# Performance work log

Hardware: AMD Instinct MI355X
Metric: run time of the kernel (lower is better)

The kernel has to match this reference:

```python
import jax, jax.numpy as jnp
import numpy as np

T = 2048          # tokens (single-sequence prefill)
HID = 4096        # hidden_size
NH = 32           # num attention heads
NKV = 8           # num kv heads (GQA)
HD = 128          # head_dim
QKV_OUT = (NH + 2 * NKV) * HD  # 6144
THETA = 10000.0
SCALING = HD ** -0.5


def setup_inputs() -> dict:
    key = jax.random.key(0)
    ks = jax.random.split(key, 8)
    positions = jnp.arange(T, dtype=jnp.int32)
    # per-token int8 quantized hidden states (symmetric, [-127,127])
    q_act = jax.random.randint(ks[0], (T, HID), -127, 128, dtype=jnp.int32)
    # per-token dynamic activation scale
    act_scale = jax.random.uniform(ks[1], (T,), jnp.float32) * 0.01 + 0.001
    # int4 weights stored unsigned [0,15] with per-output-channel scale & zero point
    w_qkv_q = jax.random.randint(ks[2], (QKV_OUT, HID), 0, 16, dtype=jnp.int32)
    w_qkv_scale = jax.random.uniform(ks[3], (QKV_OUT,), jnp.float32) * 0.01 + 0.001
    w_qkv_zero = jax.random.uniform(ks[4], (QKV_OUT,), jnp.float32) * 2.0 + 7.0
    w_o_q = jax.random.randint(ks[5], (HID, HID), 0, 16, dtype=jnp.int32)
    w_o_scale = jax.random.uniform(ks[6], (HID,), jnp.float32) * 0.01 + 0.001
    w_o_zero = jax.random.uniform(ks[7], (HID,), jnp.float32) * 2.0 + 7.0
    return dict(positions=positions, q_act=q_act, act_scale=act_scale,
                w_qkv_q=w_qkv_q, w_qkv_scale=w_qkv_scale, w_qkv_zero=w_qkv_zero,
                w_o_q=w_o_q, w_o_scale=w_o_scale, w_o_zero=w_o_zero)


def w4a8_linear(qa_f, s_a, a_sum, qw, s_w, z_w):
    # y[t,o] = s_a[t]*s_w[o] * ( (qa @ qw^T)[t,o] - z_w[o]*sum_j qa[t,j] )
    acc = jnp.matmul(qa_f, qw.astype(jnp.float32).T)  # [T, O]
    return (s_a[:, None] * s_w[None, :]) * (acc - z_w[None, :] * a_sum[:, None])


def apply_rope(x, positions):
    # neox-style RoPE over full head_dim
    half = HD // 2
    inv_freq = THETA ** (-jnp.arange(0, half, dtype=jnp.float32) / half * 1.0)
    inv_freq = 1.0 / (THETA ** (jnp.arange(0, HD, 2, dtype=jnp.float32) / HD))
    freqs = positions.astype(jnp.float32)[:, None] * inv_freq[None, :]  # [T, HD/2]
    cos = jnp.cos(freqs)[:, None, :]
    sin = jnp.sin(freqs)[:, None, :]
    x1, x2 = x[..., :half], x[..., half:]
    return jnp.concatenate([x1 * cos - x2 * sin, x2 * cos + x1 * sin], axis=-1)


def dynamic_quant_with_sum(x):
    # per-token symmetric int8 dynamic quantization + fused sum
    s = jnp.maximum(jnp.max(jnp.abs(x), axis=-1), 1e-8) / 127.0  # [T]
    q = jnp.clip(jnp.round(x / s[:, None]), -127, 127)
    return q, s, jnp.sum(q, axis=-1)


def reference(positions, q_act, act_scale, w_qkv_q, w_qkv_scale, w_qkv_zero,
              w_o_q, w_o_scale, w_o_zero):
    qa_f = q_act.astype(jnp.float32)
    a_sum = jnp.sum(qa_f, axis=-1)  # fused activation sum
    qkv = w4a8_linear(qa_f, act_scale, a_sum, w_qkv_q, w_qkv_scale, w_qkv_zero)
    q, k, v = jnp.split(qkv, [NH * HD, NH * HD + NKV * HD], axis=-1)
    q = q.reshape(T, NH, HD)
    k = k.reshape(T, NKV, HD)
    v = v.reshape(T, NKV, HD)
    q = apply_rope(q, positions)
    k = apply_rope(k, positions)
    # GQA: repeat kv heads
    rep = NH // NKV
    k = jnp.repeat(k, rep, axis=1)  # [T, NH, HD]
    v = jnp.repeat(v, rep, axis=1)
    scores = jnp.einsum('qhd,khd->hqk', q, k) * SCALING  # [NH, T, T]
    causal = jnp.tril(jnp.ones((T, T), dtype=bool))
    scores = jnp.where(causal[None], scores, -jnp.inf)
    probs = jax.nn.softmax(scores, axis=-1)
    attn = jnp.einsum('hqk,khd->qhd', probs, v).reshape(T, NH * HD)
    # invoke_quant_fuse_sum: dynamic per-token quantization of attn output
    q2, s2, sum2 = dynamic_quant_with_sum(attn)
    out = w4a8_linear(q2, s2, sum2, w_o_q, w_o_scale, w_o_zero)
    return out
```

## Files before the change

### kernel.cpp

```cpp
#include <hip/hip_runtime.h>

#define T 2048
#define HID 4096
#define NH 32
#define NKV 8
#define HD 128
#define QKV_OUT ((NH + 2*NKV) * HD)
#define SCALING 0.08838834764831843f
#define QS2 0.12751744954f
#define DEFER_THR 10.0f
#define ROPE_C 0.20762050593046014f

typedef __attribute__((ext_vector_type(8))) short bfrag;
typedef __attribute__((ext_vector_type(4))) float ffrag;
typedef __attribute__((ext_vector_type(4))) int  ifrag;
typedef __attribute__((ext_vector_type(16))) char c16;

__device__ __forceinline__ short f2bf(float f) {
  unsigned u = __builtin_bit_cast(unsigned, f);
  u += 0x7fffu + ((u >> 16) & 1u);
  return (short)(u >> 16);
}

__device__ __forceinline__ void split2(float x, short& hi, short& lo) {
  unsigned u = __builtin_bit_cast(unsigned, x);
  unsigned uh = u + (0x7fffu + ((u >> 16) & 1u));
  hi = (short)(uh >> 16);
  float fh = __builtin_bit_cast(float, uh & 0xffff0000u);
  float r = x - fh;
  unsigned ur = __builtin_bit_cast(unsigned, r);
  ur += 0x7fffu + ((ur >> 16) & 1u);
  lo = (short)(ur >> 16);
}

__device__ __forceinline__ void gload_lds16(const void* g, void* l) {
  __builtin_amdgcn_global_load_lds(
      (const __attribute__((address_space(1))) unsigned int*)g,
      (__attribute__((address_space(3))) unsigned int*)l, 16, 0, 0);
}


__global__ __launch_bounds__(256)
void asum_conv(const int* __restrict__ qact, float* __restrict__ a_sum,
               char* __restrict__ a_i8, float2* __restrict__ tab) {
  __shared__ int red[256];
  const int t = blockIdx.x, tid = threadIdx.x;
  if (t < 512) {
    int idx = t * 256 + tid;
    int p = idx >> 6, j = idx & 63;
    float fr = (float)p * exp2f(-ROPE_C * (float)j);
    float sn, cs; sincosf(fr, &sn, &cs);
    tab[idx] = make_float2(cs, sn);
  }
  const int* row = qact + (size_t)t * HID + tid * 16;
  int s = 0;
  c16 o;
#pragma unroll
  for (int i = 0; i < 4; i++) {
    int4 v = *(const int4*)(row + i * 4);
    s += v.x + v.y + v.z + v.w;
    o[i*4+0] = (char)v.x; o[i*4+1] = (char)v.y;
    o[i*4+2] = (char)v.z; o[i*4+3] = (char)v.w;
  }
  const int chunk = (tid & ~7) | ((tid & 7) ^ (t & 7));
  *(c16*)(a_i8 + (size_t)t * HID + chunk * 16) = o;
  red[tid] = s; __syncthreads();
  for (int off = 128; off > 0; off >>= 1) {
    if (tid < off) red[tid] += red[tid + off];
    __syncthreads();
  }
  if (tid == 0) a_sum[t] = (float)red[0];
}

__global__ __launch_bounds__(256)
void conv_i2c(const int* __restrict__ src, char* __restrict__ dst, int n16) {
  int idx = blockIdx.x * 256 + threadIdx.x;
  if (idx >= n16) return;
  const int4* s4 = (const int4*)src + (size_t)idx * 4;
  c16 o;
#pragma unroll
  for (int j = 0; j < 4; j++) {
    int4 v = s4[j];
    o[j*4+0] = (char)v.x; o[j*4+1] = (char)v.y;
    o[j*4+2] = (char)v.z; o[j*4+3] = (char)v.w;
  }
  const int idxp = (idx & ~7) | ((idx & 7) ^ ((idx >> 8) & 7));
  *(c16*)(dst + (size_t)idxp * 16) = o;
}

__global__ __launch_bounds__(256)
void gemm_i8(const char* __restrict__ A, const char* __restrict__ W,
             const float* __restrict__ s_a, const float* __restrict__ asum,
             const float* __restrict__ s_w, const float* __restrict__ z_w,
             float* __restrict__ C, int M, int N, int K) {
  __shared__ __align__(16) char As[2][128 * 128];
  __shared__ __align__(16) char Bs[2][128 * 128];
  const int tid = threadIdx.x;
  const int lane = tid & 63;
  const int quad = lane >> 4, l15 = lane & 15;
  const int wave = tid >> 6;
  const int wm = (wave >> 1) * 64, wn = (wave & 1) * 64;
  const int bm = blockIdx.y * 128, bn = blockIdx.x * 128;
  const int sr = tid >> 3, sc = (tid & 7) * 16;

  ifrag acc[4][4];
#pragma unroll
  for (int mi = 0; mi < 4; mi++)
#pragma unroll
    for (int ni = 0; ni < 4; ni++)
      acc[mi][ni] = (ifrag){0, 0, 0, 0};

  auto stage = [&](int k0, int b) {
#pragma unroll
    for (int j = 0; j < 4; j++) {
      gload_lds16(A + (size_t)(bm + j * 32 + sr) * K + k0 + sc,
                  &As[b][j * 4096 + tid * 16]);
      gload_lds16(W + (size_t)(bn + j * 32 + sr) * K + k0 + sc,
                  &Bs[b][j * 4096 + tid * 16]);
    }
  };

  const int scol0 = ((quad)     ^ (l15 & 7)) * 16;
  const int scol1 = ((4 + quad) ^ (l15 & 7)) * 16;

  stage(0, 0);
  asm volatile("s_waitcnt vmcnt(0)" ::: "memory");
  __builtin_amdgcn_s_barrier();

  int cur = 0;
  for (int k0 = 0; k0 < K; k0 += 128) {
    if (k0 + 128 < K) stage(k0 + 128, cur ^ 1);

#pragma unroll
    for (int ks = 0; ks < 2; ks++) {
      const int scol = ks ? scol1 : scol0;
      ifrag af[4], bfv[4];
#pragma unroll
      for (int mi = 0; mi < 4; mi++)
        af[mi] = *(const ifrag*)&As[cur][(wm + mi * 16 + l15) * 128 + scol];
#pragma unroll
      for (int ni = 0; ni < 4; ni++)
        bfv[ni] = *(const ifrag*)&Bs[cur][(wn + ni * 16 + l15) * 128 + scol];
#pragma unroll
      for (int mi = 0; mi < 4; mi++)
#pragma unroll
        for (int ni = 0; ni < 4; ni++)
          acc[mi][ni] = __builtin_amdgcn_mfma_i32_16x16x64_i8(
              af[mi], bfv[ni], acc[mi][ni], 0, 0, 0);
    }

    asm volatile("s_waitcnt vmcnt(0)" ::: "memory");
    __builtin_amdgcn_s_barrier();
    cur ^= 1;
  }

#pragma unroll
  for (int mi = 0; mi < 4; mi++) {
    int row0 = bm + wm + mi * 16 + quad * 4;
#pragma unroll
    for (int r = 0; r < 4; r++) {
      int row = row0 + r;
      float sa = s_a[row], av = asum[row];
#pragma unroll
      for (int ni = 0; ni < 4; ni++) {
        int col = bn + wn + ni * 16 + l15;
        C[(size_t)row * N + col] = (sa * s_w[col]) * ((float)acc[mi][ni][r] - z_w[col] * av);
      }
    }
  }
}

__global__ __launch_bounds__(256)
void split_kv(const float* __restrict__ qkv, const int* __restrict__ positions,
              const float2* __restrict__ tab,
              short* __restrict__ Kh, short* __restrict__ Kl,
              short* __restrict__ Vth) {
  __shared__ __align__(16) short Vh_lds[128 * 72];
  const int kvh = blockIdx.y;
  const int t0 = blockIdx.x * 64;
  const int tid = threadIdx.x;

#pragma unroll
  for (int it = 0; it < 4; it++) {
    int c = tid + 256 * it;
    int key = c >> 4, dc = c & 15;
    const int t = t0 + key;
    const float* kr = qkv + (size_t)t * QKV_OUT
                      + (size_t)NH * HD + (size_t)kvh * HD;
    float4 a = *(const float4*)(kr + dc * 4);
    float4 b = *(const float4*)(kr + dc * 4 + 64);
    float av[4] = {a.x, a.y, a.z, a.w};
    float bv[4] = {b.x, b.y, b.z, b.w};
    const float2* tr = tab + (size_t)positions[t] * 64 + dc * 4;
    short4 ha, la, hb, lb;
    short hh, ll;
#pragma unroll
    for (int jj = 0; jj < 4; jj++) {
      float cs = tr[jj].x, sn = tr[jj].y;
      float x1 = av[jj], x2 = bv[jj];
      float r1 = x1 * cs - x2 * sn;
      float r2 = x2 * cs + x1 * sn;
      split2(r1, hh, ll); ((short*)&ha)[jj] = hh; ((short*)&la)[jj] = ll;
      split2(r2, hh, ll); ((short*)&hb)[jj] = hh; ((short*)&lb)[jj] = ll;
    }
    const int uu = ((dc >> 1) ^ t) & 7;
    const int h4 = (dc & 1) * 4;
    size_t base = (size_t)kvh * T * HD + (size_t)t * HD;
    *(short4*)(Kh + base + uu * 8 + h4) = ha;
    *(short4*)(Kl + base + uu * 8 + h4) = la;
    *(short4*)(Kh + base + (8 + uu) * 8 + h4) = hb;
    *(short4*)(Kl + base + (8 + uu) * 8 + h4) = lb;
  }
#pragma unroll
  for (int i = 0; i < 8; i++) {
    int c = tid + 256 * i;
    int key = c >> 5, dc = c & 31;
    float4 f = *(const float4*)(qkv + (size_t)(t0 + key) * QKV_OUT
                                + (size_t)(NH + NKV) * HD + (size_t)kvh * HD + dc * 4);
    Vh_lds[(dc*4+0)*72 + key] = f2bf(f.x);
    Vh_lds[(dc*4+1)*72 + key] = f2bf(f.y);
    Vh_lds[(dc*4+2)*72 + key] = f2bf(f.z);
    Vh_lds[(dc*4+3)*72 + key] = f2bf(f.w);
  }
  __syncthreads();
#pragma unroll
  for (int i = 0; i < 2; i++) {
    int c = tid + 256 * i;
    int row = c >> 2, cc = c & 3;
    int sd = (row >> 1) & 3;
    size_t o = (size_t)kvh * HD * T + (size_t)row * T + t0 + ((cc ^ sd)) * 8;
    *(bfrag*)(Vth + o) = *(const bfrag*)&Vh_lds[row * 72 + cc * 8];
  }
#pragma unroll
  for (int i = 0; i < 2; i++) {
    int c = tid + 256 * i;
    int row = c >> 2, cc = c & 3;
    int sd = (row >> 1) & 3;
    size_t o = (size_t)kvh * HD * T + (size_t)row * T + t0 + 32 + ((cc ^ sd)) * 8;
    *(bfrag*)(Vth + o) = *(const bfrag*)&Vh_lds[row * 72 + 32 + cc * 8];
  }
}

__global__ __launch_bounds__(256)
void attn_kernel(const float* __restrict__ qkv, const int* __restrict__ positions,
                 const float2* __restrict__ tab,
                 const short* __restrict__ Kh, const short* __restrict__ Kl,
                 const short* __restrict__ Vth,
                 float* __restrict__ attn) {
  __shared__ __align__(16) short Ksh[2][32 * 128];
  __shared__ __align__(16) short Ksl[2][32 * 128];
  __shared__ __align__(16) short Vsh[2][128 * 32];
  __shared__ __align__(16) short Psh[4 * 16 * 40];

  const int kvh = blockIdx.x & 7;
  const int pair = blockIdx.x >> 3;
  const int tid = threadIdx.x;
  const int lane = tid & 63;
  const int wv = tid >> 6;
  const int l15 = lane & 15, quad = lane >> 4;
  const int h = kvh * 4 + wv;
  short* Pw = Psh + wv * 16 * 40;

  const short* KhB = Kh + (size_t)kvh * T * HD;
  const short* KlB = Kl + (size_t)kvh * T * HD;
  const short* VhB = Vth + (size_t)kvh * HD * T;

  const int offK0 = (tid >> 4) * 128 + (tid & 15) * 8;
  const int offK1 = offK0 + 16 * 128;
  const int offV0 = (tid >> 2) * T + (tid & 3) * 8;
  const int offV1 = offV0 + 64 * T;
  const int wv1k = wv * 1024;

  auto stage = [&](int k0, int b) {
    const short* khs = KhB + (size_t)k0 * HD;
    const short* kls = KlB + (size_t)k0 * HD;
    const short* vs  = VhB + k0;
    gload_lds16(khs + offK0, (char*)&Ksh[b][0] + wv1k);
    gload_lds16(khs + offK1, (char*)&Ksh[b][0] + 4096 + wv1k);
    gload_lds16(kls + offK0, (char*)&Ksl[b][0] + wv1k);
    gload_lds16(kls + offK1, (char*)&Ksl[b][0] + 4096 + wv1k);
    gload_lds16(vs + offV0, (char*)&Vsh[b][0] + wv1k);
    gload_lds16(vs + offV1, (char*)&Vsh[b][0] + 4096 + wv1k);
  };

  const int sdv = (l15 >> 1) & 3;
  const int vq8 = (quad ^ sdv) * 8;
  int uuk[4];
#pragma unroll
  for (int kc = 0; kc < 4; kc++) {
    int s = 4 * kc + quad;
    uuk[kc] = ((s & 8) | ((s ^ l15) & 7)) * 8;
  }

  bfrag ones;
#pragma unroll
  for (int j = 0; j < 8; j++) ones[j] = (short)0x3f80;

  for (int pass = 0; pass < 2; pass++) {
    const int qt = pass ? pair : 127 - pair;
    const int q0 = qt * 16;
    const int nk = (q0 >> 5) + 1;

    bfrag qh[4], ql[4];
    {
      const float* qrow = qkv + (size_t)(q0 + l15) * QKV_OUT + (size_t)h * HD;
      float fvv[4][8];
#pragma unroll
      for (int kc = 0; kc < 4; kc++) {
        float4 f0 = *(const float4*)(qrow + kc * 32 + quad * 8);
        float4 f1 = *(const float4*)(qrow + kc * 32 + quad * 8 + 4);
        fvv[kc][0] = f0.x; fvv[kc][1] = f0.y; fvv[kc][2] = f0.z; fvv[kc][3] = f0.w;
        fvv[kc][4] = f1.x; fvv[kc][5] = f1.y; fvv[kc][6] = f1.z; fvv[kc][7] = f1.w;
      }
      const float2* trw = tab + (size_t)positions[q0 + l15] * 64;
#pragma unroll
      for (int kc = 0; kc < 2; kc++) {
#pragma unroll
        for (int j = 0; j < 8; j++) {
          int d = kc * 32 + quad * 8 + j;
          float2 cssn = trw[d];
          float x1 = fvv[kc][j], x2 = fvv[kc + 2][j];
          fvv[kc][j]     = x1 * cssn.x - x2 * cssn.y;
          fvv[kc + 2][j] = x2 * cssn.x + x1 * cssn.y;
        }
      }
#pragma unroll
      for (int kc = 0; kc < 4; kc++)
#pragma unroll
        for (int j = 0; j < 8; j++) {
          short hi, lo; split2(fvv[kc][j] * QS2, hi, lo);
          qh[kc][j] = hi; ql[kc][j] = lo;
        }
    }

    ffrag o[8], ol;
    ol = (ffrag){0.f, 0.f, 0.f, 0.f};
#pragma unroll
    for (int n = 0; n < 8; n++) o[n] = (ffrag){0.f, 0.f, 0.f, 0.f};
    float m_i[4] = {-1e30f, -1e30f, -1e30f, -1e30f};

    auto compute_tile = [&](int k0, int b, bool maskq) {
      const short* ksh = &Ksh[b][0];
      const short* ksl = &Ksl[b][0];
      const short* vsh = &Vsh[b][0];
      ffrag s[2];
      s[0] = (ffrag){0.f,0.f,0.f,0.f}; s[1] = (ffrag){0.f,0.f,0.f,0.f};
#pragma unroll
      for (int kc = 0; kc < 4; kc++) {
#pragma unroll
        for (int n = 0; n < 2; n++) {
          const int rb = (n * 16 + l15) * 128 + uuk[kc];
          bfrag bh = *(const bfrag*)&ksh[rb];
          bfrag bl = *(const bfrag*)&ksl[rb];
          s[n] = __builtin_amdgcn_mfma_f32_16x16x32_bf16(qh[kc], bh, s[n], 0,0,0);
          s[n] = __builtin_amdgcn_mfma_f32_16x16x32_bf16(qh[kc], bl, s[n], 0,0,0);
          s[n] = __builtin_amdgcn_mfma_f32_16x16x32_bf16(ql[kc], bh, s[n], 0,0,0);
        }
      }
      float sv[2][4];
#pragma unroll
      for (int n = 0; n < 2; n++)
#pragma unroll
        for (int r = 0; r < 4; r++) {
          float v = s[n][r];
          if (maskq) {
            int key = k0 + n * 16 + l15;
            int row = q0 + quad * 4 + r;
            if (key > row) v = -1e30f;
          }
          sv[n][r] = v;
        }
      float lm[4];
      bool trig = false;
#pragma unroll
      for (int r = 0; r < 4; r++) {
        lm[r] = fmaxf(sv[0][r], sv[1][r]);
        trig = trig || (lm[r] > m_i[r] + DEFER_THR);
      }
      if (__any(trig)) {
#pragma unroll
        for (int r = 0; r < 4; r++) {
          float m2 = lm[r];
          m2 = fmaxf(m2, __shfl_xor(m2, 1));
          m2 = fmaxf(m2, __shfl_xor(m2, 2));
          m2 = fmaxf(m2, __shfl_xor(m2, 4));
          m2 = fmaxf(m2, __shfl_xor(m2, 8));
          float mn = fmaxf(m_i[r], m2);
          float a = exp2f(m_i[r] - mn);
          m_i[r] = mn;
          ol[r] *= a;
#pragma unroll
          for (int n = 0; n < 8; n++) o[n][r] *= a;
        }
      }
#pragma unroll
      for (int n = 0; n < 2; n++)
#pragma unroll
        for (int r = 0; r < 4; r++) {
          float p = exp2f(sv[n][r] - m_i[r]);
          Pw[(quad*4 + r) * 40 + n*16 + l15] = f2bf(p);
        }
      bfrag ph = *(const bfrag*)&Pw[l15 * 40 + quad * 8];
      ol = __builtin_amdgcn_mfma_f32_16x16x32_bf16(ph, ones, ol, 0,0,0);
#pragma unroll
      for (int n = 0; n < 8; n++) {
        bfrag vh = *(const bfrag*)&vsh[(n * 16 + l15) * 32 + vq8];
        o[n] = __builtin_amdgcn_mfma_f32_16x16x32_bf16(ph, vh, o[n], 0,0,0);
      }
    };

    stage(0, 0);
    asm volatile("s_waitcnt vmcnt(0)" ::: "memory");
    __builtin_amdgcn_s_barrier();

    int cur = 0;
    for (int kt = 0; kt < nk - 1; kt++) {
      const int k0 = kt << 5;
      stage(k0 + 32, cur ^ 1);
      compute_tile(k0, cur, false);
      asm volatile("s_waitcnt vmcnt(0)" ::: "memory");
      __builtin_amdgcn_s_barrier();
      cur ^= 1;
    }
    compute_tile((nk - 1) << 5, cur, true);
    __builtin_amdgcn_s_barrier();

    float inv[4];
#pragma unroll
    for (int r = 0; r < 4; r++) inv[r] = 1.f / ol[r];
#pragma unroll
    for (int n = 0; n < 8; n++)
#pragma unroll
      for (int r = 0; r < 4; r++) {
        int row = q0 + quad * 4 + r;
        attn[(size_t)row * HID + (size_t)h * HD + n * 16 + l15] = o[n][r] * inv[r];
      }
  }
}

__global__ __launch_bounds__(256)
void quant_kernel(const float* __restrict__ x, char* __restrict__ q2,
                  float* __restrict__ s2, float* __restrict__ sum2) {
  __shared__ float red[256];
  const int t = blockIdx.x, tid = threadIdx.x;
  const float* row = x + (size_t)t * HID;
  float4 v[4];
  float m = 0.f;
#pragma unroll
  for (int i = 0; i < 4; i++) {
    v[i] = *(const float4*)(row + tid * 16 + i * 4);
    m = fmaxf(m, fmaxf(fmaxf(fabsf(v[i].x), fabsf(v[i].y)),
                       fmaxf(fabsf(v[i].z), fabsf(v[i].w))));
  }
  red[tid] = m; __syncthreads();
  for (int off = 128; off > 0; off >>= 1) {
    if (tid < off) red[tid] = fmaxf(red[tid], red[tid + off]);
    __syncthreads();
  }
  float s = fmaxf(red[0], 1e-8f) / 127.f;
  __syncthreads();
  float ssum = 0.f;
  c16 o;
#pragma unroll
  for (int i = 0; i < 4; i++) {
    float q;
    q = fminf(127.f, fmaxf(-127.f, rintf(v[i].x / s))); ssum += q; o[i*4+0] = (char)(int)q;
    q = fminf(127.f, fmaxf(-127.f, rintf(v[i].y / s))); ssum += q; o[i*4+1] = (char)(int)q;
    q = fminf(127.f, fmaxf(-127.f, rintf(v[i].z / s))); ssum += q; o[i*4+2] = (char)(int)q;
    q = fminf(127.f, fmaxf(-127.f, rintf(v[i].w / s))); ssum += q; o[i*4+3] = (char)(int)q;
  }
  const int chunk = (tid & ~7) | ((tid & 7) ^ (t & 7));
  *(c16*)(q2 + (size_t)t * HID + chunk * 16) = o;
  red[tid] = ssum; __syncthreads();
  for (int off = 128; off > 0; off >>= 1) {
    if (tid < off) red[tid] += red[tid + off];
    __syncthreads();
  }
  if (tid == 0) { s2[t] = s; sum2[t] = red[0]; }
}

extern "C" void kernel_launch(void* const* d_in, const int* in_sizes, int n_in,
                              void* d_out, int out_size, void* d_ws, size_t ws_size,
                              hipStream_t stream) {
  const int*   positions   = (const int*)d_in[0];
  const int*   q_act       = (const int*)d_in[1];
  const float* act_scale   = (const float*)d_in[2];
  const int*   w_qkv_q     = (const int*)d_in[3];
  const float* w_qkv_scale = (const float*)d_in[4];
  const float* w_qkv_zero  = (const float*)d_in[5];
  const int*   w_o_q       = (const int*)d_in[6];
  const float* w_o_scale   = (const float*)d_in[7];
  const float* w_o_zero    = (const float*)d_in[8];
  float* out = (float*)d_out;

  size_t off = 0;
  auto alloc = [&](size_t bytes) -> void* {
    void* p = (char*)d_ws + off;
    off += (bytes + 255) & ~(size_t)255;
    return p;
  };
  float* qkv   = (float*)alloc((size_t)T * QKV_OUT * 4);
  char*  act8  = (char*)alloc((size_t)T * HID);
  char*  w8    = (char*)alloc((size_t)QKV_OUT * HID);
  short* Kh    = (short*)alloc((size_t)NKV * T * HD * 2);
  short* Kl    = (short*)alloc((size_t)NKV * T * HD * 2);
  short* Vth   = (short*)alloc((size_t)NKV * T * HD * 2);
  float* a_sum = (float*)alloc(T * 4);
  float* s2    = (float*)alloc(T * 4);
  float* sum2  = (float*)alloc(T * 4);
  float2* tab  = (float2*)alloc((size_t)T * 64 * 8);
  (void)ws_size;

  asum_conv<<<T, 256, 0, stream>>>(q_act, a_sum, act8, tab);
  conv_i2c<<<(QKV_OUT * HID / 16 + 255) / 256, 256, 0, stream>>>(
      w_qkv_q, w8, QKV_OUT * HID / 16);
  gemm_i8<<<dim3(QKV_OUT / 128, T / 128), 256, 0, stream>>>(
      act8, w8, act_scale, a_sum, w_qkv_scale, w_qkv_zero, qkv, T, QKV_OUT, HID);
  split_kv<<<dim3(T / 64, NKV), 256, 0, stream>>>(
      qkv, positions, tab, Kh, Kl, Vth);
  attn_kernel<<<dim3(512), 256, 0, stream>>>(
      qkv, positions, tab, Kh, Kl, Vth, out);
  conv_i2c<<<(HID * HID / 16 + 255) / 256, 256, 0, stream>>>(
      w_o_q, w8, HID * HID / 16);
  quant_kernel<<<T, 256, 0, stream>>>(out, act8, s2, sum2);
  gemm_i8<<<dim3(HID / 128, T / 128), 256, 0, stream>>>(
      act8, w8, s2, sum2, w_o_scale, w_o_zero, out, T, HID, HID);
}
```

Before: 467.0 us.

## Fold weight conversions into prep kernels and split attention into single-tile blocks

Both int32-to-int8 weight conversion launches are removed. Their blocks are appended to the activation-prep kernel and to the K/V split kernel, so each conversion runs alongside other memory-bound work instead of as its own launch. The attention kernel no longer has each block process a paired long and short query tile in two passes. It now launches 1024 blocks, one query tile each, ordered heaviest first. This aims to cut launch count and serial gaps and improve scheduling granularity, but it gives up the explicit pairwise load balancing and relies on the hardware block scheduler.

```diff
diff --git a/kernel.cpp b/kernel.cpp
--- a/kernel.cpp
+++ b/kernel.cpp
@@ -41,10 +41,28 @@
 
 
 __global__ __launch_bounds__(256)
-void asum_conv(const int* __restrict__ qact, float* __restrict__ a_sum,
-               char* __restrict__ a_i8, float2* __restrict__ tab) {
+void prep_a(const int* __restrict__ qact, float* __restrict__ a_sum,
+            char* __restrict__ a_i8, float2* __restrict__ tab,
+            const int* __restrict__ wsrc, char* __restrict__ wdst) {
   __shared__ int red[256];
-  const int t = blockIdx.x, tid = threadIdx.x;
+  const int bid = blockIdx.x, tid = threadIdx.x;
+
+  if (bid >= T) {
+    int idx = (bid - T) * 256 + tid;
+    const int4* s4 = (const int4*)wsrc + (size_t)idx * 4;
+    c16 o;
+#pragma unroll
+    for (int j = 0; j < 4; j++) {
+      int4 v = s4[j];
+      o[j*4+0] = (char)v.x; o[j*4+1] = (char)v.y;
+      o[j*4+2] = (char)v.z; o[j*4+3] = (char)v.w;
+    }
+    const int idxp = (idx & ~7) | ((idx & 7) ^ ((idx >> 8) & 7));
+    *(c16*)(wdst + (size_t)idxp * 16) = o;
+    return;
+  }
+
+  const int t = bid;
   if (t < 512) {
     int idx = t * 256 + tid;
     int p = idx >> 6, j = idx & 63;
@@ -70,22 +88,6 @@
     __syncthreads();
   }
   if (tid == 0) a_sum[t] = (float)red[0];
-}
-
-__global__ __launch_bounds__(256)
-void conv_i2c(const int* __restrict__ src, char* __restrict__ dst, int n16) {
-  int idx = blockIdx.x * 256 + threadIdx.x;
-  if (idx >= n16) return;
-  const int4* s4 = (const int4*)src + (size_t)idx * 4;
-  c16 o;
-#pragma unroll
-  for (int j = 0; j < 4; j++) {
-    int4 v = s4[j];
-    o[j*4+0] = (char)v.x; o[j*4+1] = (char)v.y;
-    o[j*4+2] = (char)v.z; o[j*4+3] = (char)v.w;
-  }
-  const int idxp = (idx & ~7) | ((idx & 7) ^ ((idx >> 8) & 7));
-  *(c16*)(dst + (size_t)idxp * 16) = o;
 }
 
 __global__ __launch_bounds__(256)
@@ -171,14 +173,31 @@
 }
 
 __global__ __launch_bounds__(256)
-void split_kv(const float* __restrict__ qkv, const int* __restrict__ positions,
-              const float2* __restrict__ tab,
-              short* __restrict__ Kh, short* __restrict__ Kl,
-              short* __restrict__ Vth) {
+void kv_prep(const float* __restrict__ qkv, const int* __restrict__ positions,
+             const float2* __restrict__ tab,
+             short* __restrict__ Kh, short* __restrict__ Kl,
+             short* __restrict__ Vth,
+             const int* __restrict__ wsrc, char* __restrict__ wdst) {
   __shared__ __align__(16) short Vh_lds[128 * 72];
-  const int kvh = blockIdx.y;
-  const int t0 = blockIdx.x * 64;
-  const int tid = threadIdx.x;
+  const int bid = blockIdx.x, tid = threadIdx.x;
+
+  if (bid >= 256) {
+    int idx = (bid - 256) * 256 + tid;
+    const int4* s4 = (const int4*)wsrc + (size_t)idx * 4;
+    c16 o;
+#pragma unroll
+    for (int j = 0; j < 4; j++) {
+      int4 v = s4[j];
+      o[j*4+0] = (char)v.x; o[j*4+1] = (char)v.y;
+      o[j*4+2] = (char)v.z; o[j*4+3] = (char)v.w;
+    }
+    const int idxp = (idx & ~7) | ((idx & 7) ^ ((idx >> 8) & 7));
+    *(c16*)(wdst + (size_t)idxp * 16) = o;
+    return;
+  }
+
+  const int kvh = bid & 7;
+  const int t0 = (bid >> 3) * 64;
 
 #pragma unroll
   for (int it = 0; it < 4; it++) {
@@ -253,7 +272,7 @@
   __shared__ __align__(16) short Psh[4 * 16 * 40];
 
   const int kvh = blockIdx.x & 7;
-  const int pair = blockIdx.x >> 3;
+  const int qt  = 127 - (int)(blockIdx.x >> 3);
   const int tid = threadIdx.x;
   const int lane = tid & 63;
   const int wv = tid >> 6;
@@ -296,146 +315,142 @@
 #pragma unroll
   for (int j = 0; j < 8; j++) ones[j] = (short)0x3f80;
 
-  for (int pass = 0; pass < 2; pass++) {
-    const int qt = pass ? pair : 127 - pair;
-    const int q0 = qt * 16;
-    const int nk = (q0 >> 5) + 1;
-
-    bfrag qh[4], ql[4];
-    {
-      const float* qrow = qkv + (size_t)(q0 + l15) * QKV_OUT + (size_t)h * HD;
-      float fvv[4][8];
-#pragma unroll
-      for (int kc = 0; kc < 4; kc++) {
-        float4 f0 = *(const float4*)(qrow + kc * 32 + quad * 8);
-        float4 f1 = *(const float4*)(qrow + kc * 32 + quad * 8 + 4);
-        fvv[kc][0] = f0.x; fvv[kc][1] = f0.y; fvv[kc][2] = f0.z; fvv[kc][3] = f0.w;
-        fvv[kc][4] = f1.x; fvv[kc][5] = f1.y; fvv[kc][6] = f1.z; fvv[kc][7] = f1.w;
-      }
-      const float2* trw = tab + (size_t)positions[q0 + l15] * 64;
-#pragma unroll
-      for (int kc = 0; kc < 2; kc++) {
-#pragma unroll
-        for (int j = 0; j < 8; j++) {
-          int d = kc * 32 + quad * 8 + j;
-          float2 cssn = trw[d];
-          float x1 = fvv[kc][j], x2 = fvv[kc + 2][j];
-          fvv[kc][j]     = x1 * cssn.x - x2 * cssn.y;
-          fvv[kc + 2][j] = x2 * cssn.x + x1 * cssn.y;
+  const int q0 = qt * 16;
+  const int nk = (q0 >> 5) + 1;
+
+  bfrag qh[4], ql[4];
+  {
+    const float* qrow = qkv + (size_t)(q0 + l15) * QKV_OUT + (size_t)h * HD;
+    float fvv[4][8];
+#pragma unroll
+    for (int kc = 0; kc < 4; kc++) {
+      float4 f0 = *(const float4*)(qrow + kc * 32 + quad * 8);
+      float4 f1 = *(const float4*)(qrow + kc * 32 + quad * 8 + 4);
+      fvv[kc][0] = f0.x; fvv[kc][1] = f0.y; fvv[kc][2] = f0.z; fvv[kc][3] = f0.w;
+      fvv[kc][4] = f1.x; fvv[kc][5] = f1.y; fvv[kc][6] = f1.z; fvv[kc][7] = f1.w;
+    }
+    const float2* trw = tab + (size_t)positions[q0 + l15] * 64;
+#pragma unroll
+    for (int kc = 0; kc < 2; kc++) {
+#pragma unroll
+      for (int j = 0; j < 8; j++) {
+        int d = kc * 32 + quad * 8 + j;
+        float2 cssn = trw[d];
+        float x1 = fvv[kc][j], x2 = fvv[kc + 2][j];
+        fvv[kc][j]     = x1 * cssn.x - x2 * cssn.y;
+        fvv[kc + 2][j] = x2 * cssn.x + x1 * cssn.y;
+      }
+    }
+#pragma unroll
+    for (int kc = 0; kc < 4; kc++)
+#pragma unroll
+      for (int j = 0; j < 8; j++) {
+        short hi, lo; split2(fvv[kc][j] * QS2, hi, lo);
+        qh[kc][j] = hi; ql[kc][j] = lo;
+      }
+  }
+
+  ffrag o[8], ol;
+  ol = (ffrag){0.f, 0.f, 0.f, 0.f};
+#pragma unroll
+  for (int n = 0; n < 8; n++) o[n] = (ffrag){0.f, 0.f, 0.f, 0.f};
+  float m_i[4] = {-1e30f, -1e30f, -1e30f, -1e30f};
+
+  auto compute_tile = [&](int k0, int b, bool maskq) {
+    const short* ksh = &Ksh[b][0];
+    const short* ksl = &Ksl[b][0];
+    const short* vsh = &Vsh[b][0];
+    ffrag s[2];
+    s[0] = (ffrag){0.f,0.f,0.f,0.f}; s[1] = (ffrag){0.f,0.f,0.f,0.f};
+#pragma unroll
+    for (int kc = 0; kc < 4; kc++) {
+#pragma unroll
+      for (int n = 0; n < 2; n++) {
+        const int rb = (n * 16 + l15) * 128 + uuk[kc];
+        bfrag bh = *(const bfrag*)&ksh[rb];
+        bfrag bl = *(const bfrag*)&ksl[rb];
+        s[n] = __builtin_amdgcn_mfma_f32_16x16x32_bf16(qh[kc], bh, s[n], 0,0,0);
+        s[n] = __builtin_amdgcn_mfma_f32_16x16x32_bf16(qh[kc], bl, s[n], 0,0,0);
+        s[n] = __builtin_amdgcn_mfma_f32_16x16x32_bf16(ql[kc], bh, s[n], 0,0,0);
+      }
+    }
+    float sv[2][4];
+#pragma unroll
+    for (int n = 0; n < 2; n++)
+#pragma unroll
+      for (int r = 0; r < 4; r++) {
+        float v = s[n][r];
+        if (maskq) {
+          int key = k0 + n * 16 + l15;
+          int row = q0 + quad * 4 + r;
+          if (key > row) v = -1e30f;
         }
-      }
-#pragma unroll
-      for (int kc = 0; kc < 4; kc++)
-#pragma unroll
-        for (int j = 0; j < 8; j++) {
-          short hi, lo; split2(fvv[kc][j] * QS2, hi, lo);
-          qh[kc][j] = hi; ql[kc][j] = lo;
-        }
-    }
-
-    ffrag o[8], ol;
-    ol = (ffrag){0.f, 0.f, 0.f, 0.f};
-#pragma unroll
-    for (int n = 0; n < 8; n++) o[n] = (ffrag){0.f, 0.f, 0.f, 0.f};
-    float m_i[4] = {-1e30f, -1e30f, -1e30f, -1e30f};
-
-    auto compute_tile = [&](int k0, int b, bool maskq) {
-      const short* ksh = &Ksh[b][0];
-      const short* ksl = &Ksl[b][0];
-      const short* vsh = &Vsh[b][0];
-      ffrag s[2];
-      s[0] = (ffrag){0.f,0.f,0.f,0.f}; s[1] = (ffrag){0.f,0.f,0.f,0.f};
-#pragma unroll
-      for (int kc = 0; kc < 4; kc++) {
-#pragma unroll
-        for (int n = 0; n < 2; n++) {
-          const int rb = (n * 16 + l15) * 128 + uuk[kc];
-          bfrag bh = *(const bfrag*)&ksh[rb];
-          bfrag bl = *(const bfrag*)&ksl[rb];
-          s[n] = __builtin_amdgcn_mfma_f32_16x16x32_bf16(qh[kc], bh, s[n], 0,0,0);
-          s[n] = __builtin_amdgcn_mfma_f32_16x16x32_bf16(qh[kc], bl, s[n], 0,0,0);
-          s[n] = __builtin_amdgcn_mfma_f32_16x16x32_bf16(ql[kc], bh, s[n], 0,0,0);
-        }
-      }
-      float sv[2][4];
-#pragma unroll
-      for (int n = 0; n < 2; n++)
-#pragma unroll
-        for (int r = 0; r < 4; r++) {
-          float v = s[n][r];
-          if (maskq) {
-            int key = k0 + n * 16 + l15;
-            int row = q0 + quad * 4 + r;
-            if (key > row) v = -1e30f;
-          }
-          sv[n][r] = v;
-        }
-      float lm[4];
-      bool trig = false;
+        sv[n][r] = v;
+      }
+    float lm[4];
+    bool trig = false;
+#pragma unroll
+    for (int r = 0; r < 4; r++) {
+      lm[r] = fmaxf(sv[0][r], sv[1][r]);
+      trig = trig || (lm[r] > m_i[r] + DEFER_THR);
+    }
+    if (__any(trig)) {
 #pragma unroll
       for (int r = 0; r < 4; r++) {
-        lm[r] = fmaxf(sv[0][r], sv[1][r]);
-        trig = trig || (lm[r] > m_i[r] + DEFER_THR);
-      }
-      if (__any(trig)) {
-#pragma unroll
-        for (int r = 0; r < 4; r++) {
-          float m2 = lm[r];
-          m2 = fmaxf(m2, __shfl_xor(m2, 1));
-          m2 = fmaxf(m2, __shfl_xor(m2, 2));
-          m2 = fmaxf(m2, __shfl_xor(m2, 4));
-          m2 = fmaxf(m2, __shfl_xor(m2, 8));
-          float mn = fmaxf(m_i[r], m2);
-          float a = exp2f(m_i[r] - mn);
-          m_i[r] = mn;
-          ol[r] *= a;
-#pragma unroll
-          for (int n = 0; n < 8; n++) o[n][r] *= a;
-        }
-      }
-#pragma unroll
-      for (int n = 0; n < 2; n++)
-#pragma unroll
-        for (int r = 0; r < 4; r++) {
-          float p = exp2f(sv[n][r] - m_i[r]);
-          Pw[(quad*4 + r) * 40 + n*16 + l15] = f2bf(p);
-        }
-      bfrag ph = *(const bfrag*)&Pw[l15 * 40 + quad * 8];
-      ol = __builtin_amdgcn_mfma_f32_16x16x32_bf16(ph, ones, ol, 0,0,0);
-#pragma unroll
-      for (int n = 0; n < 8; n++) {
-        bfrag vh = *(const bfrag*)&vsh[(n * 16 + l15) * 32 + vq8];
-        o[n] = __builtin_amdgcn_mfma_f32_16x16x32_bf16(ph, vh, o[n], 0,0,0);
-      }
-    };
-
-    stage(0, 0);
+        float m2 = lm[r];
+        m2 = fmaxf(m2, __shfl_xor(m2, 1));
+        m2 = fmaxf(m2, __shfl_xor(m2, 2));
+        m2 = fmaxf(m2, __shfl_xor(m2, 4));
+        m2 = fmaxf(m2, __shfl_xor(m2, 8));
+        float mn = fmaxf(m_i[r], m2);
+        float a = exp2f(m_i[r] - mn);
+        m_i[r] = mn;
+        ol[r] *= a;
+#pragma unroll
+        for (int n = 0; n < 8; n++) o[n][r] *= a;
+      }
+    }
+#pragma unroll
+    for (int n = 0; n < 2; n++)
+#pragma unroll
+      for (int r = 0; r < 4; r++) {
+        float p = exp2f(sv[n][r] - m_i[r]);
+        Pw[(quad*4 + r) * 40 + n*16 + l15] = f2bf(p);
+      }
+    bfrag ph = *(const bfrag*)&Pw[l15 * 40 + quad * 8];
+    ol = __builtin_amdgcn_mfma_f32_16x16x32_bf16(ph, ones, ol, 0,0,0);
+#pragma unroll
+    for (int n = 0; n < 8; n++) {
+      bfrag vh = *(const bfrag*)&vsh[(n * 16 + l15) * 32 + vq8];
+      o[n] = __builtin_amdgcn_mfma_f32_16x16x32_bf16(ph, vh, o[n], 0,0,0);
+    }
+  };
+
+  stage(0, 0);
+  asm volatile("s_waitcnt vmcnt(0)" ::: "memory");
+  __builtin_amdgcn_s_barrier();
+
+  int cur = 0;
+  for (int kt = 0; kt < nk - 1; kt++) {
+    const int k0 = kt << 5;
+    stage(k0 + 32, cur ^ 1);
+    compute_tile(k0, cur, false);
     asm volatile("s_waitcnt vmcnt(0)" ::: "memory");
     __builtin_amdgcn_s_barrier();
-
-    int cur = 0;
-    for (int kt = 0; kt < nk - 1; kt++) {
-      const int k0 = kt << 5;
-      stage(k0 + 32, cur ^ 1);
-      compute_tile(k0, cur, false);
-      asm volatile("s_waitcnt vmcnt(0)" ::: "memory");
-      __builtin_amdgcn_s_barrier();
-      cur ^= 1;
-    }
-    compute_tile((nk - 1) << 5, cur, true);
-    __builtin_amdgcn_s_barrier();
-
-    float inv[4];
-#pragma unroll
-    for (int r = 0; r < 4; r++) inv[r] = 1.f / ol[r];
-#pragma unroll
-    for (int n = 0; n < 8; n++)
-#pragma unroll
-      for (int r = 0; r < 4; r++) {
-        int row = q0 + quad * 4 + r;
-        attn[(size_t)row * HID + (size_t)h * HD + n * 16 + l15] = o[n][r] * inv[r];
-      }
-  }
+    cur ^= 1;
+  }
+  compute_tile((nk - 1) << 5, cur, true);
+
+  float inv[4];
+#pragma unroll
+  for (int r = 0; r < 4; r++) inv[r] = 1.f / ol[r];
+#pragma unroll
+  for (int n = 0; n < 8; n++)
+#pragma unroll
+    for (int r = 0; r < 4; r++) {
+      int row = q0 + quad * 4 + r;
+      attn[(size_t)row * HID + (size_t)h * HD + n * 16 + l15] = o[n][r] * inv[r];
+    }
 }
 
 __global__ __launch_bounds__(256)
@@ -511,17 +526,14 @@
   float2* tab  = (float2*)alloc((size_t)T * 64 * 8);
   (void)ws_size;
 
-  asum_conv<<<T, 256, 0, stream>>>(q_act, a_sum, act8, tab);
-  conv_i2c<<<(QKV_OUT * HID / 16 + 255) / 256, 256, 0, stream>>>(
-      w_qkv_q, w8, QKV_OUT * HID / 16);
+  prep_a<<<T + QKV_OUT * HID / 16 / 256, 256, 0, stream>>>(
+      q_act, a_sum, act8, tab, w_qkv_q, w8);
   gemm_i8<<<dim3(QKV_OUT / 128, T / 128), 256, 0, stream>>>(
       act8, w8, act_scale, a_sum, w_qkv_scale, w_qkv_zero, qkv, T, QKV_OUT, HID);
-  split_kv<<<dim3(T / 64, NKV), 256, 0, stream>>>(
-      qkv, positions, tab, Kh, Kl, Vth);
-  attn_kernel<<<dim3(512), 256, 0, stream>>>(
+  kv_prep<<<256 + HID * HID / 16 / 256, 256, 0, stream>>>(
+      qkv, positions, tab, Kh, Kl, Vth, w_o_q, w8);
+  attn_kernel<<<dim3(1024), 256, 0, stream>>>(
       qkv, positions, tab, Kh, Kl, Vth, out);
-  conv_i2c<<<(HID * HID / 16 + 255) / 256, 256, 0, stream>>>(
-      w_o_q, w8, HID * HID / 16);
   quant_kernel<<<T, 256, 0, stream>>>(out, act8, s2, sum2);
   gemm_i8<<<dim3(HID / 128, T / 128), 256, 0, stream>>>(
       act8, w8, s2, sum2, w_o_scale, w_o_zero, out, T, HID, HID);
```

New measurement: 463.7 us. Within noise of the previous version (-0.7%).
